# Kernel tuning notes

Hardware: AMD Instinct MI355X
Metric: run time of the kernel (lower is better)

The kernel has to match this reference:

```python
import jax, jax.numpy as jnp
import numpy as np

INSIZE = 512
OUTSIZE = 512
N_U = 64
N_V = 64
SIGMA_MIN = 0.1
SIGMA_MAX = 1.0
BATCH = 8192


def setup_inputs() -> dict:
    key = jax.random.key(0)
    kx, kp, ku, kv, kb = jax.random.split(key, 5)
    x = jax.random.normal(kx, (BATCH, INSIZE), dtype=jnp.float32)
    nsigma = min(INSIZE, OUTSIZE)
    p = 0.001 * jax.random.normal(kp, (nsigma,), dtype=jnp.float32)
    U = jnp.triu(jax.random.normal(ku, (INSIZE, INSIZE), dtype=jnp.float32))
    V = jnp.triu(jax.random.normal(kv, (OUTSIZE, OUTSIZE), dtype=jnp.float32))
    bound = 1.0 / float(np.sqrt(INSIZE))
    bias = jax.random.uniform(kb, (1, OUTSIZE), minval=-bound, maxval=bound, dtype=jnp.float32)
    return {"x": x, "p": p, "U": U, "V": V, "bias": bias}


def _house_chain(x, rows):
    # Sequentially apply Householder reflections. rows[i] has its leading
    # entries zeroed (upper-triangular structure), which makes the full-width
    # dot/outer-product exactly equal to torch's Hprod on the trailing slice
    # u[-k:] while leaving the leading columns of x untouched.
    def step(x, u):
        alpha = 2.0 * (x @ u) / jnp.dot(u, u)  # [B]
        return x - alpha[:, None] * u[None, :], None
    x, _ = jax.lax.scan(step, x, rows)
    return x


def _sigma_matrix(p, dtype):
    r = (SIGMA_MAX - SIGMA_MIN) / 2.0
    sigma_mean = SIGMA_MIN + r
    sigmas = 2.0 * r * (jax.nn.sigmoid(p) - 0.5) + sigma_mean  # [nsigma]
    nsigma = min(INSIZE, OUTSIZE)
    idx = jnp.arange(nsigma)
    return jnp.zeros((INSIZE, OUTSIZE), dtype=dtype).at[idx, idx].set(sigmas.astype(dtype))


def reference(x, p, U, V, bias):
    # Umultiply: i = 0 .. N_U-1, reflector U[i] with k = insize - i
    x = _house_chain(x, jnp.triu(U)[:N_U])
    # x @ Sigma (rectangular diagonal of constrained singular values)
    x = x @ _sigma_matrix(p, x.dtype)
    # Vmultiply: i = N_V-1 down to 0, reflector V[i] with k = outsize - i
    x = _house_chain(x, jnp.triu(V)[:N_V][::-1])
    return x + bias
```

## Files before the change

### kernel.cpp

```cpp
#include <hip/hip_runtime.h>
#include <hip/hip_bf16.h>
#include <math.h>


#define INSIZE 512
#define NREF 64
#define BATCH 8192

static constexpr int OFF_WT    = 0;
static constexpr int OFF_SIGMA = 131072;
static constexpr int OFF_BETAU = OFF_SIGMA + 512;
static constexpr int OFF_BETAV = OFF_BETAU + 64;
static constexpr int OFF_GU    = OFF_BETAV + 64;
static constexpr int OFF_GV    = OFF_GU + 4096;
static constexpr int OFF_C     = OFF_GV + 4096;

__device__ inline float sigma_of(float pv) {
    float s = 1.0f / (1.0f + expf(-pv));
    return 0.55f + 0.9f * (s - 0.5f);
}

__global__ __launch_bounds__(256) void k_prep(const float* __restrict__ U,
                                              const float* __restrict__ V,
                                              const float* __restrict__ p,
                                              float* __restrict__ ws) {
    int b = blockIdx.x, t = threadIdx.x;
    if (b == 192) {
        for (int c = t; c < INSIZE; c += 256)
            (ws + OFF_SIGMA)[c] = sigma_of(p[c]);
        return;
    }
    __shared__ float rowi[INSIZE];
    int w = t >> 6, l = t & 63;
    if (b < 128) {
        bool isV = (b >= 64);
        int i = isV ? (b - 64) : b;
        const float* src = isV ? V : U;
        int srow = isV ? (63 - i) : i;
        for (int c = t; c < INSIZE; c += 256) rowi[c] = src[srow * INSIZE + c];
        __syncthreads();
        float* G = ws + (isV ? OFF_GV : OFF_GU);
        float* beta = ws + (isV ? OFF_BETAV : OFF_BETAU);
        for (int jj = 0; jj < 16; ++jj) {
            int j = w * 16 + jj;
            int jrow = isV ? (63 - j) : j;
            const float* rj = src + jrow * INSIZE;
            float s = 0.f;
            for (int c = l; c < INSIZE; c += 64) s += rowi[c] * rj[c];
            for (int o = 32; o > 0; o >>= 1) s += __shfl_down(s, o, 64);
            if (l == 0) {
                bool keep = isV ? (j < i) : (j > i);
                G[i * 64 + j] = keep ? s : 0.0f;
                if (j == i) beta[i] = 2.0f / s;
            }
        }
    } else {
        int i = b - 128;
        for (int c = t; c < INSIZE; c += 256)
            rowi[c] = U[i * INSIZE + c] * sigma_of(p[c]);
        __syncthreads();
        float* C = ws + OFF_C;
        for (int jj = 0; jj < 16; ++jj) {
            int j = w * 16 + jj;
            const float* rj = V + (63 - j) * INSIZE;
            float s = 0.f;
            for (int c = l; c < INSIZE; c += 64) s += rowi[c] * rj[c];
            for (int o = 32; o > 0; o >>= 1) s += __shfl_down(s, o, 64);
            if (l == 0) C[i * 64 + j] = s;
        }
    }
}

__global__ __launch_bounds__(256) void k_WtE(const float* __restrict__ U,
                                             const float* __restrict__ V,
                                             float* __restrict__ ws) {
    __shared__ float Ps[128][34];
    __shared__ float Qs[128][34];
    __shared__ float Xs[4160];
    int t = threadIdx.x;
    int r0 = (blockIdx.x >> 4) * 32;
    int c0 = (blockIdx.x & 15) * 32;
    const float* sig = ws + OFF_SIGMA;
    float* Qf = &Qs[0][0];

    for (int i = t; i < 1024; i += 256) {
        *(float4*)&Xs[i * 4] = *(const float4*)&(ws + OFF_GU)[i * 4];
        *(float4*)&Qf[i * 4] = *(const float4*)&(ws + OFF_GV)[i * 4];
    }
    if (t < 64) {
        Xs[4096 + t] = (ws + OFF_BETAU)[t];
        Qf[4096 + t] = (ws + OFF_BETAV)[t];
    }
    __syncthreads();

    int l = t & 63;
    int c_loc = (t >> 6) * 8 + (l >> 3);
    int grp = l & 7;
    int srcbase = l & 0x38;
    float pj[8], pr[8];
    {
        int r = r0 + c_loc;
#pragma unroll
        for (int jj = 0; jj < 8; ++jj) pj[jj] = U[(grp * 8 + jj) * INSIZE + r];
#pragma unroll
        for (int m = 0; m < 64; ++m) {
            float tmp = pj[m & 7] * Xs[4096 + m];
            float am = __shfl(tmp, srcbase | (m >> 3), 64);
            if (grp == (m >> 3)) pj[m & 7] = am;
#pragma unroll
            for (int jj = 0; jj < 8; ++jj)
                pj[jj] -= am * Xs[m * 64 + grp * 8 + jj];
        }
#pragma unroll
        for (int jj = 0; jj < 8; ++jj) Ps[grp * 8 + jj][c_loc] = pj[jj];
    }
    {
        int c = c0 + c_loc;
#pragma unroll
        for (int ii = 0; ii < 8; ++ii)
            pr[ii] = V[(63 - (grp * 8 + ii)) * INSIZE + c];
#pragma unroll
        for (int i = 63; i >= 0; --i) {
            float tmp = pr[i & 7] * Qf[4096 + i];
            float ai = __shfl(tmp, srcbase | (i >> 3), 64);
            if (grp == (i >> 3)) pr[i & 7] = ai;
#pragma unroll
            for (int ii = 0; ii < 8; ++ii)
                pr[ii] -= ai * Qf[i * 64 + grp * 8 + ii];
        }
    }
    __syncthreads();

    for (int i = t; i < 1024; i += 256)
        *(float4*)&Xs[i * 4] = *(const float4*)&(ws + OFF_C)[i * 4];
    int lr = t & 31, kb = t >> 5;
    float sc = sig[c0 + lr];
#pragma unroll
    for (int ii = 0; ii < 8; ++ii) {
        int k = kb + ii * 8;
        Qs[k][lr] = U[k * INSIZE + c0 + lr] * sc;
    }
#pragma unroll
    for (int ii = 0; ii < 8; ++ii)
        Qs[64 + grp * 8 + ii][c_loc] = pr[ii];
    __syncthreads();

    float sr = sig[r0 + lr];
#pragma unroll
    for (int ii = 0; ii < 8; ++ii) {
        int j = kb * 8 + ii;
        float e = sr * V[(63 - j) * INSIZE + r0 + lr];
#pragma unroll 8
        for (int i = 0; i < 64; ++i)
            e -= Ps[i][lr] * Xs[i * 64 + j];
        Ps[64 + j][lr] = e;
    }
    __syncthreads();

    int ty = t >> 4, tx = t & 15;
    float a00 = 0.f, a01 = 0.f, a10 = 0.f, a11 = 0.f;
#pragma unroll
    for (int k = 0; k < 128; ++k) {
        float2 a = *(const float2*)&Ps[k][ty * 2];
        float2 bq = *(const float2*)&Qs[k][tx * 2];
        a00 += a.x * bq.x; a01 += a.x * bq.y;
        a10 += a.y * bq.x; a11 += a.y * bq.y;
    }
    int rg = r0 + ty * 2, cg = c0 + tx * 2;
    float w00 = ((rg == cg) ? sig[rg] : 0.f) - a00;
    float w01 = ((rg == cg + 1) ? sig[rg] : 0.f) - a01;
    float w10 = ((rg + 1 == cg) ? sig[rg + 1] : 0.f) - a10;
    float w11 = ((rg + 1 == cg + 1) ? sig[rg + 1] : 0.f) - a11;
    unsigned short* Wt = (unsigned short*)(ws + OFF_WT);
    __hip_bfloat162 lo = __float22bfloat162_rn(make_float2(w00, w10));
    __hip_bfloat162 hi = __float22bfloat162_rn(make_float2(w01, w11));
    *(__hip_bfloat162*)&Wt[cg * INSIZE + rg] = lo;
    *(__hip_bfloat162*)&Wt[(cg + 1) * INSIZE + rg] = hi;
}

typedef __attribute__((ext_vector_type(8))) short short8;
typedef __attribute__((ext_vector_type(4))) float float4v;

__global__ __launch_bounds__(256) void k_gemm(const float* __restrict__ X,
                                              const float* __restrict__ ws,
                                              const float* __restrict__ bias,
                                              float* __restrict__ out) {
    __shared__ float As[64 * 32];
    __shared__ unsigned short Bs[64 * 32];
    const unsigned short* Wt = (const unsigned short*)(ws + OFF_WT);

    int L = blockIdx.x;
    int inner = L & 7;
    int bn = (L >> 3) & 7;
    int bm = (L >> 6) * 8 + inner;
    int row0 = bm * 64, col0 = bn * 64;

    int t = threadIdx.x;
    int l = t & 63, w = t >> 6;
    int wm = (w & 1) * 32, wn = (w >> 1) * 32;

    float4v acc[2][2] = {};
    int quad = l >> 4;
    int lan = l & 15;

    for (int k0 = 0; k0 < INSIZE; k0 += 32) {
        __syncthreads();
#pragma unroll
        for (int i = 0; i < 2; ++i) {
            int P = i * 256 + t;
            int prow = P >> 3, pc = P & 7;
            int lc = pc ^ (prow & 7);
            const float* g = X + (size_t)(row0 + prow) * INSIZE + k0 + lc * 4;
            __builtin_amdgcn_global_load_lds(
                (const __attribute__((address_space(1))) void*)g,
                (__attribute__((address_space(3))) void*)(As + P * 4), 16, 0, 0);
        }
        {
            int P = t;
            int prow = P >> 2, pc = P & 3;
            int lc = pc ^ ((prow >> 1) & 3);
            const unsigned short* g = Wt + (size_t)(col0 + prow) * INSIZE + k0 + lc * 8;
            __builtin_amdgcn_global_load_lds(
                (const __attribute__((address_space(1))) void*)g,
                (__attribute__((address_space(3))) void*)(Bs + P * 8), 16, 0, 0);
        }
        __syncthreads();

        short8 af[2];
        short8 bf[2];
#pragma unroll
        for (int mi = 0; mi < 2; ++mi) {
            int rl = wm + mi * 16 + lan;
            int c0q = quad * 2;
            const float4v lo = *(const float4v*)(As + (rl * 8 + (c0q ^ (rl & 7))) * 4);
            const float4v hi = *(const float4v*)(As + (rl * 8 + ((c0q + 1) ^ (rl & 7))) * 4);
            union { short8 s; __hip_bfloat162 h[4]; } u;
            u.h[0] = __float22bfloat162_rn(make_float2(lo[0], lo[1]));
            u.h[1] = __float22bfloat162_rn(make_float2(lo[2], lo[3]));
            u.h[2] = __float22bfloat162_rn(make_float2(hi[0], hi[1]));
            u.h[3] = __float22bfloat162_rn(make_float2(hi[2], hi[3]));
            af[mi] = u.s;
        }
#pragma unroll
        for (int ni = 0; ni < 2; ++ni) {
            int rn = wn + ni * 16 + lan;
            int c = quad ^ ((rn >> 1) & 3);
            bf[ni] = *(const short8*)(Bs + (rn * 4 + c) * 8);
        }
#pragma unroll
        for (int mi = 0; mi < 2; ++mi)
#pragma unroll
            for (int ni = 0; ni < 2; ++ni)
                acc[mi][ni] = __builtin_amdgcn_mfma_f32_16x16x32_bf16(
                    af[mi], bf[ni], acc[mi][ni], 0, 0, 0);
    }

#pragma unroll
    for (int ni = 0; ni < 2; ++ni) {
        int c = col0 + wn + ni * 16 + lan;
        float bv = bias[c];
#pragma unroll
        for (int mi = 0; mi < 2; ++mi) {
            int rbase = row0 + wm + mi * 16 + quad * 4;
#pragma unroll
            for (int r = 0; r < 4; ++r)
                out[(size_t)(rbase + r) * INSIZE + c] = acc[mi][ni][r] + bv;
        }
    }
}

extern "C" void kernel_launch(void* const* d_in, const int* in_sizes, int n_in,
                              void* d_out, int out_size, void* d_ws, size_t ws_size,
                              hipStream_t stream) {
    const float* x    = (const float*)d_in[0];
    const float* p    = (const float*)d_in[1];
    const float* U    = (const float*)d_in[2];
    const float* V    = (const float*)d_in[3];
    const float* bias = (const float*)d_in[4];
    float* ws  = (float*)d_ws;
    float* out = (float*)d_out;

    k_prep<<<193, 256, 0, stream>>>(U, V, p, ws);
    k_WtE<<<256, 256, 0, stream>>>(U, V, ws);
    k_gemm<<<1024, 256, 0, stream>>>(x, ws, bias, out);
}
```

Measured before the change: 113.6 us.

## Double GEMM K-tile to 64 and vectorize prep dot products via registers

The GEMM kernel now stages a 64-wide K slice of X and Wt per iteration instead of 32, with new XOR swizzles, and runs two MFMA sub-steps per tile. This halves the number of barrier pairs and load rounds. The prep kernel drops the shared-memory row staging and its barrier, loading float4 pairs straight into registers and reducing them with an 8-wide dot product. The cost is more LDS per block (24KB vs 12KB), which may reduce occupancy.

```diff
diff --git a/kernel.cpp b/kernel.cpp
--- a/kernel.cpp
+++ b/kernel.cpp
@@ -18,6 +18,11 @@
 __device__ inline float sigma_of(float pv) {
     float s = 1.0f / (1.0f + expf(-pv));
     return 0.55f + 0.9f * (s - 0.5f);
+}
+
+__device__ inline float dot8(float4 a0, float4 a1, float4 b0, float4 b1) {
+    return a0.x * b0.x + a0.y * b0.y + a0.z * b0.z + a0.w * b0.w
+         + a1.x * b1.x + a1.y * b1.y + a1.z * b1.z + a1.w * b1.w;
 }
 
 __global__ __launch_bounds__(256) void k_prep(const float* __restrict__ U,
@@ -30,23 +35,22 @@
             (ws + OFF_SIGMA)[c] = sigma_of(p[c]);
         return;
     }
-    __shared__ float rowi[INSIZE];
     int w = t >> 6, l = t & 63;
+    float4 b0, b1;
     if (b < 128) {
         bool isV = (b >= 64);
         int i = isV ? (b - 64) : b;
         const float* src = isV ? V : U;
         int srow = isV ? (63 - i) : i;
-        for (int c = t; c < INSIZE; c += 256) rowi[c] = src[srow * INSIZE + c];
-        __syncthreads();
+        const float4* ri4 = (const float4*)(src + srow * INSIZE);
+        b0 = ri4[l * 2]; b1 = ri4[l * 2 + 1];
         float* G = ws + (isV ? OFF_GV : OFF_GU);
         float* beta = ws + (isV ? OFF_BETAV : OFF_BETAU);
         for (int jj = 0; jj < 16; ++jj) {
             int j = w * 16 + jj;
             int jrow = isV ? (63 - j) : j;
-            const float* rj = src + jrow * INSIZE;
-            float s = 0.f;
-            for (int c = l; c < INSIZE; c += 64) s += rowi[c] * rj[c];
+            const float4* rj4 = (const float4*)(src + jrow * INSIZE);
+            float s = dot8(rj4[l * 2], rj4[l * 2 + 1], b0, b1);
             for (int o = 32; o > 0; o >>= 1) s += __shfl_down(s, o, 64);
             if (l == 0) {
                 bool keep = isV ? (j < i) : (j > i);
@@ -56,15 +60,19 @@
         }
     } else {
         int i = b - 128;
-        for (int c = t; c < INSIZE; c += 256)
-            rowi[c] = U[i * INSIZE + c] * sigma_of(p[c]);
-        __syncthreads();
+        const float4* ui4 = (const float4*)(U + i * INSIZE);
+        const float4* p4 = (const float4*)p;
+        float4 u0 = ui4[l * 2], u1 = ui4[l * 2 + 1];
+        float4 p0 = p4[l * 2], p1 = p4[l * 2 + 1];
+        b0.x = u0.x * sigma_of(p0.x); b0.y = u0.y * sigma_of(p0.y);
+        b0.z = u0.z * sigma_of(p0.z); b0.w = u0.w * sigma_of(p0.w);
+        b1.x = u1.x * sigma_of(p1.x); b1.y = u1.y * sigma_of(p1.y);
+        b1.z = u1.z * sigma_of(p1.z); b1.w = u1.w * sigma_of(p1.w);
         float* C = ws + OFF_C;
         for (int jj = 0; jj < 16; ++jj) {
             int j = w * 16 + jj;
-            const float* rj = V + (63 - j) * INSIZE;
-            float s = 0.f;
-            for (int c = l; c < INSIZE; c += 64) s += rowi[c] * rj[c];
+            const float4* rj4 = (const float4*)(V + (63 - j) * INSIZE);
+            float s = dot8(rj4[l * 2], rj4[l * 2 + 1], b0, b1);
             for (int o = 32; o > 0; o >>= 1) s += __shfl_down(s, o, 64);
             if (l == 0) C[i * 64 + j] = s;
         }
@@ -185,8 +193,8 @@
                                               const float* __restrict__ ws,
                                               const float* __restrict__ bias,
                                               float* __restrict__ out) {
-    __shared__ float As[64 * 32];
-    __shared__ unsigned short Bs[64 * 32];
+    __shared__ float As[64 * 64];
+    __shared__ unsigned short Bs[64 * 64];
     const unsigned short* Wt = (const unsigned short*)(ws + OFF_WT);
 
     int L = blockIdx.x;
@@ -203,22 +211,23 @@
     int quad = l >> 4;
     int lan = l & 15;
 
-    for (int k0 = 0; k0 < INSIZE; k0 += 32) {
+    for (int k0 = 0; k0 < INSIZE; k0 += 64) {
         __syncthreads();
+#pragma unroll
+        for (int i = 0; i < 4; ++i) {
+            int P = i * 256 + t;
+            int prow = P >> 4, pc = P & 15;
+            int lc = pc ^ (prow & 15);
+            const float* g = X + (size_t)(row0 + prow) * INSIZE + k0 + lc * 4;
+            __builtin_amdgcn_global_load_lds(
+                (const __attribute__((address_space(1))) void*)g,
+                (__attribute__((address_space(3))) void*)(As + P * 4), 16, 0, 0);
+        }
 #pragma unroll
         for (int i = 0; i < 2; ++i) {
             int P = i * 256 + t;
             int prow = P >> 3, pc = P & 7;
             int lc = pc ^ (prow & 7);
-            const float* g = X + (size_t)(row0 + prow) * INSIZE + k0 + lc * 4;
-            __builtin_amdgcn_global_load_lds(
-                (const __attribute__((address_space(1))) void*)g,
-                (__attribute__((address_space(3))) void*)(As + P * 4), 16, 0, 0);
-        }
-        {
-            int P = t;
-            int prow = P >> 2, pc = P & 3;
-            int lc = pc ^ ((prow >> 1) & 3);
             const unsigned short* g = Wt + (size_t)(col0 + prow) * INSIZE + k0 + lc * 8;
             __builtin_amdgcn_global_load_lds(
                 (const __attribute__((address_space(1))) void*)g,
@@ -226,33 +235,36 @@
         }
         __syncthreads();
 
-        short8 af[2];
-        short8 bf[2];
-#pragma unroll
-        for (int mi = 0; mi < 2; ++mi) {
-            int rl = wm + mi * 16 + lan;
-            int c0q = quad * 2;
-            const float4v lo = *(const float4v*)(As + (rl * 8 + (c0q ^ (rl & 7))) * 4);
-            const float4v hi = *(const float4v*)(As + (rl * 8 + ((c0q + 1) ^ (rl & 7))) * 4);
-            union { short8 s; __hip_bfloat162 h[4]; } u;
-            u.h[0] = __float22bfloat162_rn(make_float2(lo[0], lo[1]));
-            u.h[1] = __float22bfloat162_rn(make_float2(lo[2], lo[3]));
-            u.h[2] = __float22bfloat162_rn(make_float2(hi[0], hi[1]));
-            u.h[3] = __float22bfloat162_rn(make_float2(hi[2], hi[3]));
-            af[mi] = u.s;
-        }
-#pragma unroll
-        for (int ni = 0; ni < 2; ++ni) {
-            int rn = wn + ni * 16 + lan;
-            int c = quad ^ ((rn >> 1) & 3);
-            bf[ni] = *(const short8*)(Bs + (rn * 4 + c) * 8);
-        }
-#pragma unroll
-        for (int mi = 0; mi < 2; ++mi)
-#pragma unroll
-            for (int ni = 0; ni < 2; ++ni)
-                acc[mi][ni] = __builtin_amdgcn_mfma_f32_16x16x32_bf16(
-                    af[mi], bf[ni], acc[mi][ni], 0, 0, 0);
+#pragma unroll
+        for (int ki = 0; ki < 2; ++ki) {
+            short8 af[2];
+            short8 bf[2];
+#pragma unroll
+            for (int mi = 0; mi < 2; ++mi) {
+                int rl = wm + mi * 16 + lan;
+                int c0q = ki * 8 + quad * 2;
+                const float4v lo = *(const float4v*)(As + (rl * 16 + (c0q ^ (rl & 15))) * 4);
+                const float4v hi = *(const float4v*)(As + (rl * 16 + ((c0q + 1) ^ (rl & 15))) * 4);
+                union { short8 s; __hip_bfloat162 h[4]; } u;
+                u.h[0] = __float22bfloat162_rn(make_float2(lo[0], lo[1]));
+                u.h[1] = __float22bfloat162_rn(make_float2(lo[2], lo[3]));
+                u.h[2] = __float22bfloat162_rn(make_float2(hi[0], hi[1]));
+                u.h[3] = __float22bfloat162_rn(make_float2(hi[2], hi[3]));
+                af[mi] = u.s;
+            }
+#pragma unroll
+            for (int ni = 0; ni < 2; ++ni) {
+                int rn = wn + ni * 16 + lan;
+                int c = (ki * 4 + quad) ^ (rn & 7);
+                bf[ni] = *(const short8*)(Bs + (rn * 8 + c) * 8);
+            }
+#pragma unroll
+            for (int mi = 0; mi < 2; ++mi)
+#pragma unroll
+                for (int ni = 0; ni < 2; ++ni)
+                    acc[mi][ni] = __builtin_amdgcn_mfma_f32_16x16x32_bf16(
+                        af[mi], bf[ni], acc[mi][ni], 0, 0, 0);
+        }
     }
 
 #pragma unroll
```

Result: faster. 111.2 us, median of 2 (-2.2%).
